# Kernel optimization log

Hardware: AMD Instinct MI355X
Metric: run time of the kernel (lower is better)

Reference implementation:

```python
import jax, jax.numpy as jnp
import numpy as np

# Block-diagonal SplitMLP: fc1 group g sees [day | items[g]]; fc2 is purely per-group.
B, C, V, H, O, G = 128, 16, 32, 64, 4, 10000


def setup_inputs() -> dict:
    key = jax.random.key(0)
    ks = jax.random.split(key, 7)
    bound1 = 1.0 / np.sqrt(C + V * G)   # nn.Linear init bound for fc1 (full fan-in)
    bound2 = 1.0 / np.sqrt(H * G)       # fc2 fan-in
    return {
        "day": jax.random.normal(ks[0], (B, C), jnp.float32),
        "items": jax.random.normal(ks[1], (B, G, V), jnp.float32),
        "W1_day": jax.random.uniform(ks[2], (G, H, C), jnp.float32, -bound1, bound1),
        "W1_var": jax.random.uniform(ks[3], (G, H, V), jnp.float32, -bound1, bound1),
        "b1": jax.random.uniform(ks[4], (G, H), jnp.float32, -bound1, bound1),
        "W2": jax.random.uniform(ks[5], (G, O, H), jnp.float32, -bound2, bound2),
        "b2": jax.random.uniform(ks[6], (G, O), jnp.float32, -bound2, bound2),
    }


def reference(day, items, W1_day, W1_var, b1, W2, b2):
    # fc1: shared day columns + per-group var block, then ReLU
    h = (
        jnp.einsum("bc,ghc->bgh", day, W1_day)
        + jnp.einsum("bgv,ghv->bgh", items, W1_var)
        + b1
    )
    h = jax.nn.relu(h)
    # fc2: purely block-diagonal (num_const = 0)
    y = jnp.einsum("bgh,goh->bgo", h, W2) + b2  # (B, G, O)
    return y
```

## Files before the change

### kernel.cpp

```cpp
#include <hip/hip_runtime.h>
#include <hip/hip_bf16.h>


typedef __bf16 v8bf __attribute__((ext_vector_type(8)));
typedef __bf16 v4bf __attribute__((ext_vector_type(4)));
typedef float  v4f  __attribute__((ext_vector_type(4)));

#define B_   128
#define C_   16
#define V_   32
#define H_   64
#define O_   4
#define G_   10000
#define GPB  4
#define WS_  56
#define HS_  72
#define YS_  20

__device__ __forceinline__ v4bf cvt4(float4 f) {
  v4bf r;
  r[0] = (__bf16)f.x; r[1] = (__bf16)f.y; r[2] = (__bf16)f.z; r[3] = (__bf16)f.w;
  return r;
}
__device__ __forceinline__ v8bf cvt8(float4 lo, float4 hi) {
  v8bf r;
  r[0] = (__bf16)lo.x; r[1] = (__bf16)lo.y; r[2] = (__bf16)lo.z; r[3] = (__bf16)lo.w;
  r[4] = (__bf16)hi.x; r[5] = (__bf16)hi.y; r[6] = (__bf16)hi.z; r[7] = (__bf16)hi.w;
  return r;
}
__device__ __forceinline__ v8bf gload8(const float* __restrict__ p) {
  const float4* p4 = reinterpret_cast<const float4*>(p);
  return cvt8(p4[0], p4[1]);
}

__global__ __launch_bounds__(256, 4)
void splitmlp_kernel(const float* __restrict__ day,
                     const float* __restrict__ items,
                     const float* __restrict__ W1d,
                     const float* __restrict__ W1v,
                     const float* __restrict__ b1,
                     const float* __restrict__ W2,
                     const float* __restrict__ b2,
                     float* __restrict__ out) {
  __shared__ __bf16 W1s[H_ * WS_];
  __shared__ __bf16 Hb[4][32 * HS_];
  __shared__ float  Yb[B_ * YS_];

  const int t    = threadIdx.x;
  const int g0   = blockIdx.x * GPB;
  const int w    = t >> 6;
  const int lane = t & 63;
  const int c    = lane & 15;
  const int q    = lane >> 4;
  const int wbase = w * 32;

  v8bf zf;
#pragma unroll
  for (int i = 0; i < 8; ++i) zf[i] = (__bf16)0.0f;
  const v4f zero = {0.f, 0.f, 0.f, 0.f};

  float4 pd, pv0, pv1;
  {
    const float* W1dg = W1d + (size_t)g0 * (H_ * C_);
    const float* W1vg = W1v + (size_t)g0 * (H_ * V_);
    pd  = reinterpret_cast<const float4*>(W1dg)[t];
    pv0 = reinterpret_cast<const float4*>(W1vg)[t];
    pv1 = reinterpret_cast<const float4*>(W1vg)[t + 256];
  }

#pragma unroll 1
  for (int gi = 0; gi < GPB; ++gi) {
    const int g = g0 + gi;

    __syncthreads();
    {
      const int hd = t >> 2, kd = (t & 3) << 2;
      *reinterpret_cast<v4bf*>(&W1s[hd * WS_ + kd]) = cvt4(pd);
      const int hv0 = t >> 3, kv0 = C_ + ((t & 7) << 2);
      *reinterpret_cast<v4bf*>(&W1s[hv0 * WS_ + kv0]) = cvt4(pv0);
      const int i2 = t + 256;
      const int hv1 = i2 >> 3, kv1 = C_ + ((i2 & 7) << 2);
      *reinterpret_cast<v4bf*>(&W1s[hv1 * WS_ + kv1]) = cvt4(pv1);
    }
    if (gi < GPB - 1) {
      const float* W1dn = W1d + (size_t)(g + 1) * (H_ * C_);
      const float* W1vn = W1v + (size_t)(g + 1) * (H_ * V_);
      pd  = reinterpret_cast<const float4*>(W1dn)[t];
      pv0 = reinterpret_cast<const float4*>(W1vn)[t];
      pv1 = reinterpret_cast<const float4*>(W1vn)[t + 256];
    }
    __syncthreads();

    v8bf bfrag[2][2];
#pragma unroll
    for (int nb = 0; nb < 2; ++nb) {
      const int b = wbase + nb * 16 + c;
      const float* pit = items + (size_t)b * (G_ * V_) + (size_t)g * V_;
      const float* p0 = (q < 2) ? (day + b * C_ + q * 8) : (pit + (q - 2) * 8);
      bfrag[nb][0] = gload8(p0);
      bfrag[nb][1] = (q < 2) ? gload8(pit + 16 + q * 8) : zf;
    }

    v8bf wfrag[4][2];
#pragma unroll
    for (int m = 0; m < 4; ++m) {
      const int row = (m * 16 + c) * WS_;
      wfrag[m][0] = *reinterpret_cast<const v8bf*>(&W1s[row + q * 8]);
      wfrag[m][1] = (q < 2) ? *reinterpret_cast<const v8bf*>(&W1s[row + 32 + q * 8]) : zf;
    }

    v4f acc[4][2];
#pragma unroll
    for (int m = 0; m < 4; ++m)
#pragma unroll
      for (int nb = 0; nb < 2; ++nb) acc[m][nb] = zero;
#pragma unroll
    for (int m = 0; m < 4; ++m)
#pragma unroll
      for (int nb = 0; nb < 2; ++nb) {
        acc[m][nb] = __builtin_amdgcn_mfma_f32_16x16x32_bf16(wfrag[m][0], bfrag[nb][0], acc[m][nb], 0, 0, 0);
        acc[m][nb] = __builtin_amdgcn_mfma_f32_16x16x32_bf16(wfrag[m][1], bfrag[nb][1], acc[m][nb], 0, 0, 0);
      }

#pragma unroll
    for (int m = 0; m < 4; ++m) {
      const float4 bb = *reinterpret_cast<const float4*>(b1 + (size_t)g * H_ + m * 16 + q * 4);
#pragma unroll
      for (int nb = 0; nb < 2; ++nb) {
        v4bf hv;
        hv[0] = (__bf16)fmaxf(acc[m][nb][0] + bb.x, 0.f);
        hv[1] = (__bf16)fmaxf(acc[m][nb][1] + bb.y, 0.f);
        hv[2] = (__bf16)fmaxf(acc[m][nb][2] + bb.z, 0.f);
        hv[3] = (__bf16)fmaxf(acc[m][nb][3] + bb.w, 0.f);
        *reinterpret_cast<v4bf*>(&Hb[w][(nb * 16 + c) * HS_ + m * 16 + q * 4]) = hv;
      }
    }

    v4f y[2] = {zero, zero};
#pragma unroll
    for (int kt = 0; kt < 2; ++kt) {
      const float* pw2 = W2 + (size_t)g * (O_ * H_) + c * H_ + kt * 32 + q * 8;
      v8bf w2f = (c < O_) ? gload8(pw2) : zf;
#pragma unroll
      for (int nb = 0; nb < 2; ++nb) {
        v8bf hf = *reinterpret_cast<const v8bf*>(&Hb[w][(nb * 16 + c) * HS_ + kt * 32 + q * 8]);
        y[nb] = __builtin_amdgcn_mfma_f32_16x16x32_bf16(w2f, hf, y[nb], 0, 0, 0);
      }
    }

    if (q == 0) {
      const float4 b2v = *reinterpret_cast<const float4*>(b2 + (size_t)g * O_);
#pragma unroll
      for (int nb = 0; nb < 2; ++nb) {
        const int b = wbase + nb * 16 + c;
        float4 o;
        o.x = y[nb][0] + b2v.x;
        o.y = y[nb][1] + b2v.y;
        o.z = y[nb][2] + b2v.z;
        o.w = y[nb][3] + b2v.w;
        *reinterpret_cast<float4*>(&Yb[b * YS_ + gi * 4]) = o;
      }
    }
  }

  __syncthreads();
#pragma unroll
  for (int i = t; i < 512; i += 256) {
    const int b = i >> 2, c4 = i & 3;
    const float4 v = *reinterpret_cast<const float4*>(&Yb[b * YS_ + c4 * 4]);
    *reinterpret_cast<float4*>(out + (size_t)b * (G_ * O_) + (size_t)g0 * O_ + c4 * 4) = v;
  }
}

extern "C" void kernel_launch(void* const* d_in, const int* in_sizes, int n_in,
                              void* d_out, int out_size, void* d_ws, size_t ws_size,
                              hipStream_t stream) {
  const float* day   = (const float*)d_in[0];
  const float* items = (const float*)d_in[1];
  const float* W1d   = (const float*)d_in[2];
  const float* W1v   = (const float*)d_in[3];
  const float* b1    = (const float*)d_in[4];
  const float* W2    = (const float*)d_in[5];
  const float* b2    = (const float*)d_in[6];
  float* out = (float*)d_out;
  splitmlp_kernel<<<G_ / GPB, 256, 0, stream>>>(day, items, W1d, W1v, b1, W2, b2, out);
}
```

Measured before the change: 352.3 us.

## Double-buffer per-group weights via async global-to-LDS DMA with 8 waves

Replaces the register-staged weight copy with global_load_lds DMA of fp32 W1/W2/b1 into a double-buffered, XOR-swizzled LDS slot, prefetching two groups ahead and gating each step on vmcnt plus barriers. Blocks grow to 512 threads covering 8 groups, with each wave owning 16 batch rows. The items loads are double-buffered in registers, and outputs go straight to global memory instead of being staged through LDS. The goal is to hide weight and activation load latency behind the MFMA work, at the cost of hand-tuned waitcnt values, fragile swizzle and offset math, and fp32 weights in LDS that must be converted to bf16 on every read.

```diff
diff --git a/kernel.cpp b/kernel.cpp
--- a/kernel.cpp
+++ b/kernel.cpp
@@ -12,28 +12,29 @@
 #define H_   64
 #define O_   4
 #define G_   10000
-#define GPB  4
-#define WS_  56
+#define NG   8
+#define SLOT_B  14336
+#define OFF_W1D 0
+#define OFF_W1V 4096
+#define OFF_W2  12288
+#define OFF_B1  13312
 #define HS_  72
-#define YS_  20
-
-__device__ __forceinline__ v4bf cvt4(float4 f) {
-  v4bf r;
-  r[0] = (__bf16)f.x; r[1] = (__bf16)f.y; r[2] = (__bf16)f.z; r[3] = (__bf16)f.w;
-  return r;
-}
+
+__device__ __forceinline__ void dma16(const void* g, void* l) {
+  __builtin_amdgcn_global_load_lds(
+      (const __attribute__((address_space(1))) void*)g,
+      (__attribute__((address_space(3))) void*)l, 16, 0, 0);
+}
+__device__ __forceinline__ int swz(int a) { return a ^ (((a >> 7) & 3) << 5); }
+
 __device__ __forceinline__ v8bf cvt8(float4 lo, float4 hi) {
   v8bf r;
   r[0] = (__bf16)lo.x; r[1] = (__bf16)lo.y; r[2] = (__bf16)lo.z; r[3] = (__bf16)lo.w;
   r[4] = (__bf16)hi.x; r[5] = (__bf16)hi.y; r[6] = (__bf16)hi.z; r[7] = (__bf16)hi.w;
   return r;
 }
-__device__ __forceinline__ v8bf gload8(const float* __restrict__ p) {
-  const float4* p4 = reinterpret_cast<const float4*>(p);
-  return cvt8(p4[0], p4[1]);
-}
-
-__global__ __launch_bounds__(256, 4)
+
+__global__ __launch_bounds__(512, 4)
 void splitmlp_kernel(const float* __restrict__ day,
                      const float* __restrict__ items,
                      const float* __restrict__ W1d,
@@ -42,134 +43,155 @@
                      const float* __restrict__ W2,
                      const float* __restrict__ b2,
                      float* __restrict__ out) {
-  __shared__ __bf16 W1s[H_ * WS_];
-  __shared__ __bf16 Hb[4][32 * HS_];
-  __shared__ float  Yb[B_ * YS_];
+  __shared__ __align__(1024) char Slot[2 * SLOT_B];
+  __shared__ __bf16 Hb[8][16 * HS_];
 
   const int t    = threadIdx.x;
-  const int g0   = blockIdx.x * GPB;
   const int w    = t >> 6;
   const int lane = t & 63;
   const int c    = lane & 15;
   const int q    = lane >> 4;
-  const int wbase = w * 32;
+  const int g0   = blockIdx.x * NG;
+  const int row0 = w * 16;
 
   v8bf zf;
 #pragma unroll
   for (int i = 0; i < 8; ++i) zf[i] = (__bf16)0.0f;
   const v4f zero = {0.f, 0.f, 0.f, 0.f};
 
-  float4 pd, pv0, pv1;
+  const char* jsrc[2]; size_t jstep[2]; int jlds[2];
   {
-    const float* W1dg = W1d + (size_t)g0 * (H_ * C_);
-    const float* W1vg = W1v + (size_t)g0 * (H_ * V_);
-    pd  = reinterpret_cast<const float4*>(W1dg)[t];
-    pv0 = reinterpret_cast<const float4*>(W1vg)[t];
-    pv1 = reinterpret_cast<const float4*>(W1vg)[t + 256];
+    const int jbs[2] = {w, (w + 8 < 14) ? w + 8 : w + 8 - 14};
+#pragma unroll
+    for (int i = 0; i < 2; ++i) {
+      const int jb = jbs[i];
+      const float* base; int gsb, roff, chunk;
+      if (jb < 4)        { base = W1d; gsb = H_ * C_ * 4; roff = OFF_W1D; chunk = jb; }
+      else if (jb < 12)  { base = W1v; gsb = H_ * V_ * 4; roff = OFF_W1V; chunk = jb - 4; }
+      else if (jb == 12) { base = W2;  gsb = O_ * H_ * 4; roff = OFF_W2;  chunk = 0; }
+      else               { base = b1;  gsb = H_ * 4;      roff = OFF_B1;  chunk = 0; }
+      const int x = chunk * 1024 + lane * 16;
+      const int soff = (jb == 13) ? ((lane < 16 ? lane : 15) * 16) : swz(x);
+      jsrc[i]  = (const char*)base + (size_t)g0 * gsb + soff;
+      jstep[i] = (size_t)gsb;
+      jlds[i]  = roff + chunk * 1024;
+    }
   }
-
-#pragma unroll 1
-  for (int gi = 0; gi < GPB; ++gi) {
-    const int g = g0 + gi;
-
-    __syncthreads();
+#define ISSUE_SLOT(S) {                                          \
+    char* sb_ = &Slot[((S) & 1) * SLOT_B];                       \
+    dma16(jsrc[0] + (size_t)(S) * jstep[0], sb_ + jlds[0]);      \
+    dma16(jsrc[1] + (size_t)(S) * jstep[1], sb_ + jlds[1]); }
+
+  float4 dA, dB;
+  {
+    const float* pd = day + (size_t)(row0 + c) * C_ + (q & 1) * 8;
+    dA = reinterpret_cast<const float4*>(pd)[0];
+    dB = reinterpret_cast<const float4*>(pd)[1];
+  }
+
+  const int ioff = ((q + 2) & 3) * 8;
+  const float* pit = items + (size_t)(row0 + c) * (G_ * V_) + (size_t)g0 * V_ + ioff;
+  float4 it[2][2];
+
+  ISSUE_SLOT(0);
+  it[0][0] = reinterpret_cast<const float4*>(pit)[0];
+  it[0][1] = reinterpret_cast<const float4*>(pit)[1];
+  ISSUE_SLOT(1);
+  const v8bf dayf = (q < 2) ? cvt8(dA, dB) : zf;
+
+  const int wf0_off = (q < 2) ? (OFF_W1D + swz(c * 64 + q * 32))
+                              : (OFF_W1V + swz(c * 128 + (q - 2) * 32));
+  const int wf0_ms  = (q < 2) ? 1024 : 2048;
+  const int wf1_off = OFF_W1V + swz(c * 128 + 64 + (q & 1) * 32);
+  const int w2_off0 = OFF_W2 + swz((c & 3) * 256 + q * 32);
+  const int w2_off1 = OFF_W2 + swz((c & 3) * 256 + 128 + q * 32);
+
+#pragma unroll
+  for (int gi = 0; gi < NG; ++gi) {
+    if (gi == 0 || gi == NG - 1) {
+      asm volatile("s_waitcnt vmcnt(4)" ::: "memory");
+    } else {
+      asm volatile("s_waitcnt vmcnt(6)" ::: "memory");
+    }
+    __builtin_amdgcn_s_barrier();
+    __builtin_amdgcn_sched_barrier(0);
+
+    const char* sb = &Slot[(gi & 1) * SLOT_B];
+    const float4 b2v = *reinterpret_cast<const float4*>(b2 + (size_t)(g0 + gi) * O_);
+
+    v8bf wf0[4], wf1[4], w2f[2];
+#pragma unroll
+    for (int m = 0; m < 4; ++m) {
+      const char* p = sb + wf0_off + m * wf0_ms;
+      wf0[m] = cvt8(*reinterpret_cast<const float4*>(p),
+                    *reinterpret_cast<const float4*>(p + 16));
+      const char* p1 = sb + wf1_off + m * 2048;
+      const v8bf x1 = cvt8(*reinterpret_cast<const float4*>(p1),
+                           *reinterpret_cast<const float4*>(p1 + 16));
+      wf1[m] = (q < 2) ? x1 : zf;
+    }
     {
-      const int hd = t >> 2, kd = (t & 3) << 2;
-      *reinterpret_cast<v4bf*>(&W1s[hd * WS_ + kd]) = cvt4(pd);
-      const int hv0 = t >> 3, kv0 = C_ + ((t & 7) << 2);
-      *reinterpret_cast<v4bf*>(&W1s[hv0 * WS_ + kv0]) = cvt4(pv0);
-      const int i2 = t + 256;
-      const int hv1 = i2 >> 3, kv1 = C_ + ((i2 & 7) << 2);
-      *reinterpret_cast<v4bf*>(&W1s[hv1 * WS_ + kv1]) = cvt4(pv1);
-    }
-    if (gi < GPB - 1) {
-      const float* W1dn = W1d + (size_t)(g + 1) * (H_ * C_);
-      const float* W1vn = W1v + (size_t)(g + 1) * (H_ * V_);
-      pd  = reinterpret_cast<const float4*>(W1dn)[t];
-      pv0 = reinterpret_cast<const float4*>(W1vn)[t];
-      pv1 = reinterpret_cast<const float4*>(W1vn)[t + 256];
-    }
-    __syncthreads();
-
-    v8bf bfrag[2][2];
-#pragma unroll
-    for (int nb = 0; nb < 2; ++nb) {
-      const int b = wbase + nb * 16 + c;
-      const float* pit = items + (size_t)b * (G_ * V_) + (size_t)g * V_;
-      const float* p0 = (q < 2) ? (day + b * C_ + q * 8) : (pit + (q - 2) * 8);
-      bfrag[nb][0] = gload8(p0);
-      bfrag[nb][1] = (q < 2) ? gload8(pit + 16 + q * 8) : zf;
-    }
-
-    v8bf wfrag[4][2];
+      const char* pa = sb + w2_off0;
+      const char* pb = sb + w2_off1;
+      const v8bf a0 = cvt8(*reinterpret_cast<const float4*>(pa),
+                           *reinterpret_cast<const float4*>(pa + 16));
+      const v8bf a1 = cvt8(*reinterpret_cast<const float4*>(pb),
+                           *reinterpret_cast<const float4*>(pb + 16));
+      w2f[0] = (c < O_) ? a0 : zf;
+      w2f[1] = (c < O_) ? a1 : zf;
+    }
+
+    const v8bf icf = cvt8(it[gi & 1][0], it[gi & 1][1]);
+    const v8bf blv = (q < 2) ? dayf : icf;
+    const v8bf bhv = (q < 2) ? icf : zf;
+
+    v4f acc[4];
+#pragma unroll
+    for (int m = 0; m < 4; ++m) acc[m] = zero;
 #pragma unroll
     for (int m = 0; m < 4; ++m) {
-      const int row = (m * 16 + c) * WS_;
-      wfrag[m][0] = *reinterpret_cast<const v8bf*>(&W1s[row + q * 8]);
-      wfrag[m][1] = (q < 2) ? *reinterpret_cast<const v8bf*>(&W1s[row + 32 + q * 8]) : zf;
-    }
-
-    v4f acc[4][2];
-#pragma unroll
-    for (int m = 0; m < 4; ++m)
-#pragma unroll
-      for (int nb = 0; nb < 2; ++nb) acc[m][nb] = zero;
-#pragma unroll
-    for (int m = 0; m < 4; ++m)
-#pragma unroll
-      for (int nb = 0; nb < 2; ++nb) {
-        acc[m][nb] = __builtin_amdgcn_mfma_f32_16x16x32_bf16(wfrag[m][0], bfrag[nb][0], acc[m][nb], 0, 0, 0);
-        acc[m][nb] = __builtin_amdgcn_mfma_f32_16x16x32_bf16(wfrag[m][1], bfrag[nb][1], acc[m][nb], 0, 0, 0);
-      }
+      acc[m] = __builtin_amdgcn_mfma_f32_16x16x32_bf16(wf0[m], blv, acc[m], 0, 0, 0);
+      acc[m] = __builtin_amdgcn_mfma_f32_16x16x32_bf16(wf1[m], bhv, acc[m], 0, 0, 0);
+    }
 
 #pragma unroll
     for (int m = 0; m < 4; ++m) {
-      const float4 bb = *reinterpret_cast<const float4*>(b1 + (size_t)g * H_ + m * 16 + q * 4);
-#pragma unroll
-      for (int nb = 0; nb < 2; ++nb) {
-        v4bf hv;
-        hv[0] = (__bf16)fmaxf(acc[m][nb][0] + bb.x, 0.f);
-        hv[1] = (__bf16)fmaxf(acc[m][nb][1] + bb.y, 0.f);
-        hv[2] = (__bf16)fmaxf(acc[m][nb][2] + bb.z, 0.f);
-        hv[3] = (__bf16)fmaxf(acc[m][nb][3] + bb.w, 0.f);
-        *reinterpret_cast<v4bf*>(&Hb[w][(nb * 16 + c) * HS_ + m * 16 + q * 4]) = hv;
-      }
-    }
-
-    v4f y[2] = {zero, zero};
+      const float4 bb = *reinterpret_cast<const float4*>(sb + OFF_B1 + m * 64 + q * 16);
+      v4bf hv;
+      hv[0] = (__bf16)fmaxf(acc[m][0] + bb.x, 0.f);
+      hv[1] = (__bf16)fmaxf(acc[m][1] + bb.y, 0.f);
+      hv[2] = (__bf16)fmaxf(acc[m][2] + bb.z, 0.f);
+      hv[3] = (__bf16)fmaxf(acc[m][3] + bb.w, 0.f);
+      *reinterpret_cast<v4bf*>(&Hb[w][c * HS_ + m * 16 + q * 4]) = hv;
+    }
+
+    v4f y = zero;
 #pragma unroll
     for (int kt = 0; kt < 2; ++kt) {
-      const float* pw2 = W2 + (size_t)g * (O_ * H_) + c * H_ + kt * 32 + q * 8;
-      v8bf w2f = (c < O_) ? gload8(pw2) : zf;
-#pragma unroll
-      for (int nb = 0; nb < 2; ++nb) {
-        v8bf hf = *reinterpret_cast<const v8bf*>(&Hb[w][(nb * 16 + c) * HS_ + kt * 32 + q * 8]);
-        y[nb] = __builtin_amdgcn_mfma_f32_16x16x32_bf16(w2f, hf, y[nb], 0, 0, 0);
-      }
+      const v8bf hf = *reinterpret_cast<const v8bf*>(&Hb[w][c * HS_ + kt * 32 + q * 8]);
+      y = __builtin_amdgcn_mfma_f32_16x16x32_bf16(w2f[kt], hf, y, 0, 0, 0);
     }
 
     if (q == 0) {
-      const float4 b2v = *reinterpret_cast<const float4*>(b2 + (size_t)g * O_);
-#pragma unroll
-      for (int nb = 0; nb < 2; ++nb) {
-        const int b = wbase + nb * 16 + c;
-        float4 o;
-        o.x = y[nb][0] + b2v.x;
-        o.y = y[nb][1] + b2v.y;
-        o.z = y[nb][2] + b2v.z;
-        o.w = y[nb][3] + b2v.w;
-        *reinterpret_cast<float4*>(&Yb[b * YS_ + gi * 4]) = o;
-      }
-    }
+      float4 o;
+      o.x = y[0] + b2v.x;
+      o.y = y[1] + b2v.y;
+      o.z = y[2] + b2v.z;
+      o.w = y[3] + b2v.w;
+      *reinterpret_cast<float4*>(out + (size_t)(row0 + c) * (G_ * O_) +
+                                 (size_t)(g0 + gi) * O_) = o;
+    }
+
+    if (gi < NG - 1) {
+      const float* pn = pit + (size_t)(gi + 1) * V_;
+      it[(gi + 1) & 1][0] = reinterpret_cast<const float4*>(pn)[0];
+      it[(gi + 1) & 1][1] = reinterpret_cast<const float4*>(pn)[1];
+    }
+
+    __builtin_amdgcn_s_barrier();
+    if (gi < NG - 2) ISSUE_SLOT(gi + 2);
   }
-
-  __syncthreads();
-#pragma unroll
-  for (int i = t; i < 512; i += 256) {
-    const int b = i >> 2, c4 = i & 3;
-    const float4 v = *reinterpret_cast<const float4*>(&Yb[b * YS_ + c4 * 4]);
-    *reinterpret_cast<float4*>(out + (size_t)b * (G_ * O_) + (size_t)g0 * O_ + c4 * 4) = v;
-  }
+#undef ISSUE_SLOT
 }
 
 extern "C" void kernel_launch(void* const* d_in, const int* in_sizes, int n_in,
@@ -183,5 +205,5 @@
   const float* W2    = (const float*)d_in[5];
   const float* b2    = (const float*)d_in[6];
   float* out = (float*)d_out;
-  splitmlp_kernel<<<G_ / GPB, 256, 0, stream>>>(day, items, W1d, W1v, b1, W2, b2, out);
-}
+  splitmlp_kernel<<<G_ / NG, 512, 0, stream>>>(day, items, W1d, W1v, b1, W2, b2, out);
+}
```

New measurement: 391.6 us. 11.1% more time.
